# Optimization experiments

Measured on AMD Instinct MI355X. Metric: run time of the kernel, lower is better.

The kernel has to match this reference:

```python
import jax, jax.numpy as jnp
import numpy as np

N_NODES = 100000
N_EDGES = 1600000
IN_FEATS = 128
HEADS = 4
OUT_FEATS = 16


def setup_inputs() -> dict:
    key = jax.random.key(0)
    k1, k2, k3, k4, k5 = jax.random.split(key, 5)
    x = jax.random.normal(k1, (N_NODES, IN_FEATS), dtype=jnp.float32)
    edge_index = jax.random.randint(k2, (2, N_EDGES), 0, N_NODES, dtype=jnp.int64)
    # glorot init scales
    s_w = float(np.sqrt(6.0 / (IN_FEATS + HEADS * OUT_FEATS)))
    s_a = float(np.sqrt(6.0 / (HEADS + OUT_FEATS)))
    W = jax.random.uniform(k3, (HEADS * OUT_FEATS, IN_FEATS), jnp.float32, -s_w, s_w)
    att_i = jax.random.uniform(k4, (1, HEADS, OUT_FEATS), jnp.float32, -s_a, s_a)
    att_j = jax.random.uniform(k5, (1, HEADS, OUT_FEATS), jnp.float32, -s_a, s_a)
    return {"x": x, "edge_index": edge_index, "W": W, "att_i": att_i, "att_j": att_j}


def reference(x, edge_index, W, att_i, att_j):
    N = x.shape[0]
    H, F = att_i.shape[1], att_i.shape[2]
    src = edge_index[0]  # j (source / message sender)
    dst = edge_index[1]  # i (destination / softmax segment)
    # linear projection: [N, H, F]
    h = (x @ W.T).reshape(N, H, F)
    h_j = h[src]  # [E, H, F]
    h_i = h[dst]  # [E, H, F]
    # attention logits per edge per head
    alpha = jnp.einsum('ehf,khf->eh', h_i, att_i) + jnp.einsum('ehf,khf->eh', h_j, att_j)
    alpha = jax.nn.leaky_relu(alpha, negative_slope=0.01)
    # segment softmax over incoming edges of each destination node
    amax = jax.ops.segment_max(alpha, dst, num_segments=N)  # [N, H]
    amax = jnp.where(jnp.isfinite(amax), amax, 0.0)
    ex = jnp.exp(alpha - amax[dst])
    denom = jax.ops.segment_sum(ex, dst, num_segments=N)  # [N, H]
    alpha = ex / (denom[dst] + 1e-16)
    # weighted scatter-sum aggregation
    msg = h_j * alpha[:, :, None]  # [E, H, F]
    out = jax.ops.segment_sum(msg, dst, num_segments=N)  # [N, H, F]
    return out.reshape(N, H * F)
```

## Files before the change

### kernel.cpp

```cpp
#include <hip/hip_runtime.h>

typedef __attribute__((ext_vector_type(8))) short short8;
typedef __attribute__((ext_vector_type(4))) float f32x4;

#define N_NODES 100000
#define N_EDGES 1600000
#define IN_F 128
#define OUT_ALL 64
#define HEADS 4
#define OUT_F 16
#define NTILES (N_NODES / 16)
#define BIN_BLOCKS 250
#define EPB (N_EDGES / BIN_BLOCKS)
#define TOTAL_BLOCKS 2048
#define PROJ_BLOCKS (TOTAL_BLOCKS - BIN_BLOCKS)
#define SLICE_SHIFT 8
#define SLICE_NODES 256
#define NSLICES ((N_NODES + SLICE_NODES - 1) / SLICE_NODES)
#define SEG_CAP 4608
#define QUARTER_NODES 64
#define SORT_CAP 1280

static __device__ __forceinline__ ushort f2bf(float f) {
    unsigned u = __float_as_uint(f);
    return (ushort)((u + 0x7FFF + ((u >> 16) & 1)) >> 16);
}
static __device__ __forceinline__ float bf2f(ushort b) {
    return __uint_as_float(((unsigned)b) << 16);
}
static __device__ __forceinline__ float lrelu(float v) {
    return v > 0.f ? v : 0.01f * v;
}
static __device__ __forceinline__ short8 pack_bf16x8(float4 f0, float4 f1) {
    union { unsigned u[4]; short8 s; } r;
    asm("v_cvt_pk_bf16_f32 %0, %1, %2" : "=v"(r.u[0]) : "v"(f0.x), "v"(f0.y));
    asm("v_cvt_pk_bf16_f32 %0, %1, %2" : "=v"(r.u[1]) : "v"(f0.z), "v"(f0.w));
    asm("v_cvt_pk_bf16_f32 %0, %1, %2" : "=v"(r.u[2]) : "v"(f1.x), "v"(f1.y));
    asm("v_cvt_pk_bf16_f32 %0, %1, %2" : "=v"(r.u[3]) : "v"(f1.z), "v"(f1.w));
    return r.s;
}

__global__ __launch_bounds__(256) void prep_kernel(
    const float* __restrict__ W, const float* __restrict__ att_i,
    const float* __restrict__ att_j, float* __restrict__ wiwj,
    int* __restrict__ scursor)
{
    int idx = blockIdx.x * 256 + threadIdx.x;
    if (idx < NSLICES) scursor[idx] = 0;
    if (idx >= IN_F * 8) return;
    int k = idx >> 3, c = idx & 7;
    int h = c & 3;
    const float* att = (c < 4) ? att_i : att_j;
    float s = 0.f;
    #pragma unroll
    for (int f = 0; f < 16; ++f)
        s += W[(size_t)(h * 16 + f) * IN_F + k] * att[h * OUT_F + f];
    wiwj[k * 8 + c] = s;
}

__global__ __launch_bounds__(256) void proj_bin_kernel(
    const float* __restrict__ x, const float* __restrict__ W,
    const float* __restrict__ wiwj, const int* __restrict__ ei,
    ushort* __restrict__ hb, float* __restrict__ ai, float* __restrict__ aj,
    int* __restrict__ scursor, int2* __restrict__ seg)
{
    __shared__ int cnt[NSLICES];
    __shared__ int gbase[NSLICES];
    __shared__ int run[NSLICES];
    __shared__ __align__(16) ushort xsb[16][144];

    if (blockIdx.x < BIN_BLOCKS) {
        int base = blockIdx.x * EPB;
        const int4* __restrict__ srcp = (const int4*)(ei + base);
        const int4* __restrict__ dstp = (const int4*)(ei + N_EDGES + base);
        for (int s = threadIdx.x; s < NSLICES; s += 256) { cnt[s] = 0; run[s] = 0; }
        __syncthreads();
        for (int i = threadIdx.x; i < EPB / 4; i += 256) {
            int4 d = dstp[i];
            atomicAdd(&cnt[d.x >> SLICE_SHIFT], 1);
            atomicAdd(&cnt[d.y >> SLICE_SHIFT], 1);
            atomicAdd(&cnt[d.z >> SLICE_SHIFT], 1);
            atomicAdd(&cnt[d.w >> SLICE_SHIFT], 1);
        }
        __syncthreads();
        for (int s = threadIdx.x; s < NSLICES; s += 256) {
            int c = cnt[s];
            gbase[s] = c ? atomicAdd(&scursor[s], c) : 0;
        }
        __syncthreads();
        for (int i = threadIdx.x; i < EPB / 4; i += 256) {
            int4 sv = srcp[i];
            int4 dv = dstp[i];
            int ss, p;
            ss = dv.x >> SLICE_SHIFT; p = gbase[ss] + atomicAdd(&run[ss], 1);
            if (p < SEG_CAP) seg[(size_t)ss * SEG_CAP + p] = make_int2(sv.x, dv.x);
            ss = dv.y >> SLICE_SHIFT; p = gbase[ss] + atomicAdd(&run[ss], 1);
            if (p < SEG_CAP) seg[(size_t)ss * SEG_CAP + p] = make_int2(sv.y, dv.y);
            ss = dv.z >> SLICE_SHIFT; p = gbase[ss] + atomicAdd(&run[ss], 1);
            if (p < SEG_CAP) seg[(size_t)ss * SEG_CAP + p] = make_int2(sv.z, dv.z);
            ss = dv.w >> SLICE_SHIFT; p = gbase[ss] + atomicAdd(&run[ss], 1);
            if (p < SEG_CAP) seg[(size_t)ss * SEG_CAP + p] = make_int2(sv.w, dv.w);
        }
        return;
    }

    int bproj = blockIdx.x - BIN_BLOCKS;
    const int nproj = PROJ_BLOCKS;

    int w   = threadIdx.x >> 6;
    int l   = threadIdx.x & 63;
    int col = l & 15;
    int kg  = l >> 4;

    short8 bw[4];
    #pragma unroll
    for (int m = 0; m < 4; ++m) {
        const float* wp = W + (size_t)(w * 16 + col) * IN_F + m * 32 + kg * 8;
        float4 f0 = *(const float4*)wp;
        float4 f1 = *(const float4*)(wp + 4);
        bw[m] = pack_bf16x8(f0, f1);
    }
    short8 bwd[4];
    #pragma unroll
    for (int m = 0; m < 4; ++m) {
        float v[8];
        #pragma unroll
        for (int j = 0; j < 8; ++j)
            v[j] = (col < 8) ? wiwj[(size_t)(m * 32 + kg * 8 + j) * 8 + col] : 0.f;
        bwd[m] = pack_bf16x8(float4{v[0], v[1], v[2], v[3]},
                             float4{v[4], v[5], v[6], v[7]});
    }

    int srow = threadIdx.x >> 4;
    int sc8  = threadIdx.x & 15;

    for (int t = bproj; t < NTILES; t += nproj) {
        int nodeBase = t * 16;

        __syncthreads();
        {
            const float* xp = x + (size_t)(nodeBase + srow) * IN_F + sc8 * 8;
            float4 f0 = *(const float4*)xp;
            float4 f1 = *(const float4*)(xp + 4);
            *(short8*)&xsb[srow][sc8 * 8] = pack_bf16x8(f0, f1);
        }
        __syncthreads();

        short8 a[4];
        #pragma unroll
        for (int m = 0; m < 4; ++m)
            a[m] = *(const short8*)&xsb[col][m * 32 + kg * 8];

        f32x4 acc = {0.f, 0.f, 0.f, 0.f};
        f32x4 accd = {0.f, 0.f, 0.f, 0.f};
        #pragma unroll
        for (int m = 0; m < 4; ++m) {
            acc  = __builtin_amdgcn_mfma_f32_16x16x32_bf16(a[m], bw[m],  acc,  0, 0, 0);
            accd = __builtin_amdgcn_mfma_f32_16x16x32_bf16(a[m], bwd[m], accd, 0, 0, 0);
        }

        #pragma unroll
        for (int r = 0; r < 4; ++r)
            hb[(size_t)(nodeBase + kg * 4 + r) * OUT_ALL + w * 16 + col] = f2bf(acc[r]);

        if (col < 4) {
            #pragma unroll
            for (int r = 0; r < 4; ++r)
                ai[(size_t)(nodeBase + kg * 4 + r) * HEADS + col] = accd[r];
        } else if (col < 8) {
            #pragma unroll
            for (int r = 0; r < 4; ++r)
                aj[(size_t)(nodeBase + kg * 4 + r) * HEADS + (col - 4)] = accd[r];
        }
    }
}

__global__ __launch_bounds__(512) void agg_kernel(
    const int2* __restrict__ seg, const int* __restrict__ scursor,
    const ushort* __restrict__ hb, const float* __restrict__ ai,
    const float* __restrict__ aj, float* __restrict__ out)
{
    __shared__ int staged[SORT_CAP];
    __shared__ int sorted_src[SORT_CAP];
    __shared__ int cnt[QUARTER_NODES];
    __shared__ int run[QUARTER_NODES];
    __shared__ int rowptr[QUARTER_NODES + 1];
    __shared__ int scnt_s;

    int s       = blockIdx.x >> 2;
    int quarter = blockIdx.x & 3;
    int nbase   = (s << SLICE_SHIFT) + quarter * QUARTER_NODES;
    int total = scursor[s]; if (total > SEG_CAP) total = SEG_CAP;
    const int2* sp = seg + (size_t)s * SEG_CAP;

    for (int i = threadIdx.x; i < QUARTER_NODES; i += 512) { cnt[i] = 0; run[i] = 0; }
    if (threadIdx.x == 0) scnt_s = 0;
    __syncthreads();

    int lane = threadIdx.x & 63;
    for (int i = threadIdx.x; i < total; i += 512) {
        int2 e = sp[i];
        int d = e.y & (SLICE_NODES - 1);
        bool m = (d >> 6) == quarter;
        unsigned long long mask = __ballot(m);
        if (mask) {
            int leader = (int)__ffsll((long long)mask) - 1;
            int base = 0;
            if (lane == leader)
                base = atomicAdd(&scnt_s, (int)__popcll(mask));
            base = __shfl(base, leader, 64);
            if (m) {
                int p = base + (int)__popcll(mask & ((1ull << lane) - 1ull));
                if (p < SORT_CAP) staged[p] = (e.x << 6) | (d & 63);
                atomicAdd(&cnt[d & 63], 1);
            }
        }
    }
    __syncthreads();

    if (threadIdx.x < 64) {
        int l = threadIdx.x;
        int v = cnt[l];
        int inc = v;
        #pragma unroll
        for (int d = 1; d < 64; d <<= 1) {
            int t = __shfl_up(inc, d, 64);
            if (l >= d) inc += t;
        }
        rowptr[l] = inc - v;
        if (l == 63) rowptr[64] = inc;
    }
    __syncthreads();

    int scnt = scnt_s; if (scnt > SORT_CAP) scnt = SORT_CAP;
    for (int i = threadIdx.x; i < scnt; i += 512) {
        int v = staged[i];
        int lb = v & 63;
        int p = rowptr[lb] + atomicAdd(&run[lb], 1);
        if (p < SORT_CAP) sorted_src[p] = (int)((unsigned)v >> 6);
    }
    __syncthreads();

    int g    = threadIdx.x >> 3;
    int sub  = threadIdx.x & 7;
    int head = sub >> 1;
    int node = nbase + g;
    if (node >= N_NODES) return;
    int beg = rowptr[g], end = rowptr[g + 1];
    if (end > SORT_CAP) end = SORT_CAP;
    float aiv = ai[(size_t)node * HEADS + head];
    float acc[8] = {0.f, 0.f, 0.f, 0.f, 0.f, 0.f, 0.f, 0.f};
    float den = 0.f;

    int k = beg;
    for (; k + 4 <= end; k += 4) {
        int s0 = sorted_src[k + 0];
        int s1 = sorted_src[k + 1];
        int s2 = sorted_src[k + 2];
        int s3 = sorted_src[k + 3];
        float aj0 = aj[(size_t)s0 * HEADS + head];
        float aj1 = aj[(size_t)s1 * HEADS + head];
        float aj2 = aj[(size_t)s2 * HEADS + head];
        float aj3 = aj[(size_t)s3 * HEADS + head];
        short8 h0 = *(const short8*)(hb + (size_t)s0 * OUT_ALL + sub * 8);
        short8 h1 = *(const short8*)(hb + (size_t)s1 * OUT_ALL + sub * 8);
        short8 h2 = *(const short8*)(hb + (size_t)s2 * OUT_ALL + sub * 8);
        short8 h3 = *(const short8*)(hb + (size_t)s3 * OUT_ALL + sub * 8);
        float e0 = __expf(lrelu(aiv + aj0));
        float e1 = __expf(lrelu(aiv + aj1));
        float e2 = __expf(lrelu(aiv + aj2));
        float e3 = __expf(lrelu(aiv + aj3));
        den += (e0 + e1) + (e2 + e3);
        #pragma unroll
        for (int q = 0; q < 8; ++q)
            acc[q] += e0 * bf2f((ushort)h0[q]) + e1 * bf2f((ushort)h1[q]) +
                      e2 * bf2f((ushort)h2[q]) + e3 * bf2f((ushort)h3[q]);
    }
    for (; k < end; ++k) {
        int src = sorted_src[k];
        float ex = __expf(lrelu(aiv + aj[(size_t)src * HEADS + head]));
        den += ex;
        short8 hv = *(const short8*)(hb + (size_t)src * OUT_ALL + sub * 8);
        #pragma unroll
        for (int q = 0; q < 8; ++q)
            acc[q] += ex * bf2f((ushort)hv[q]);
    }

    float inv = 1.0f / (den + 1e-16f);
    float4 o0 = {acc[0] * inv, acc[1] * inv, acc[2] * inv, acc[3] * inv};
    float4 o1 = {acc[4] * inv, acc[5] * inv, acc[6] * inv, acc[7] * inv};
    float* op = out + (size_t)node * OUT_ALL + sub * 8;
    *(float4*)op = o0;
    *(float4*)(op + 4) = o1;
}

extern "C" void kernel_launch(void* const* d_in, const int* in_sizes, int n_in,
                              void* d_out, int out_size, void* d_ws, size_t ws_size,
                              hipStream_t stream) {
    const float* x     = (const float*)d_in[0];
    const int*   ei    = (const int*)d_in[1];
    const float* W     = (const float*)d_in[2];
    const float* att_i = (const float*)d_in[3];
    const float* att_j = (const float*)d_in[4];
    float* out = (float*)d_out;

    char* ws = (char*)d_ws;
    size_t off = 0;
    auto alloc = [&](size_t bytes) {
        void* p = ws + off;
        off += (bytes + 255) & ~(size_t)255;
        return p;
    };
    ushort* hb      = (ushort*)alloc((size_t)N_NODES * OUT_ALL * 2);
    float*  ai      = (float*)alloc((size_t)N_NODES * HEADS * 4);
    float*  aj      = (float*)alloc((size_t)N_NODES * HEADS * 4);
    float*  wiwj    = (float*)alloc((size_t)IN_F * 8 * 4);
    int*    scursor = (int*)alloc((size_t)NSLICES * 4);
    int2*   seg     = (int2*)alloc((size_t)NSLICES * SEG_CAP * 8);

    prep_kernel<<<(IN_F * 8 + 255) / 256, 256, 0, stream>>>(
        W, att_i, att_j, wiwj, scursor);
    proj_bin_kernel<<<TOTAL_BLOCKS, 256, 0, stream>>>(
        x, W, wiwj, ei, hb, ai, aj, scursor, seg);
    agg_kernel<<<NSLICES * 4, 512, 0, stream>>>(seg, scursor, hb, ai, aj, out);
}
```

Before: 88.58 us.

## Make aggregation a persistent kernel with atomic work queue; prefetch next x tile

New measurement: 104.2 us. 17.6% more time.

```diff
diff --git a/kernel.cpp b/kernel.cpp
--- a/kernel.cpp
+++ b/kernel.cpp
@@ -20,6 +20,8 @@
 #define SEG_CAP 4608
 #define QUARTER_NODES 64
 #define SORT_CAP 1280
+#define NCHUNKS (NSLICES * 4)
+#define AGG_BLOCKS 1024
 
 static __device__ __forceinline__ ushort f2bf(float f) {
     unsigned u = __float_as_uint(f);
@@ -43,10 +45,11 @@
 __global__ __launch_bounds__(256) void prep_kernel(
     const float* __restrict__ W, const float* __restrict__ att_i,
     const float* __restrict__ att_j, float* __restrict__ wiwj,
-    int* __restrict__ scursor)
+    int* __restrict__ scursor, int* __restrict__ workctr)
 {
     int idx = blockIdx.x * 256 + threadIdx.x;
     if (idx < NSLICES) scursor[idx] = 0;
+    if (idx == NSLICES) *workctr = 0;
     if (idx >= IN_F * 8) return;
     int k = idx >> 3, c = idx & 7;
     int h = c & 3;
@@ -134,22 +137,31 @@
     int srow = threadIdx.x >> 4;
     int sc8  = threadIdx.x & 15;
 
+    float4 p0 = {0,0,0,0}, p1 = {0,0,0,0};
+    if (bproj < NTILES) {
+        const float* xp = x + (size_t)(bproj * 16 + srow) * IN_F + sc8 * 8;
+        p0 = *(const float4*)xp;
+        p1 = *(const float4*)(xp + 4);
+    }
+
     for (int t = bproj; t < NTILES; t += nproj) {
         int nodeBase = t * 16;
 
         __syncthreads();
-        {
-            const float* xp = x + (size_t)(nodeBase + srow) * IN_F + sc8 * 8;
-            float4 f0 = *(const float4*)xp;
-            float4 f1 = *(const float4*)(xp + 4);
-            *(short8*)&xsb[srow][sc8 * 8] = pack_bf16x8(f0, f1);
-        }
+        *(short8*)&xsb[srow][sc8 * 8] = pack_bf16x8(p0, p1);
         __syncthreads();
 
         short8 a[4];
         #pragma unroll
         for (int m = 0; m < 4; ++m)
             a[m] = *(const short8*)&xsb[col][m * 32 + kg * 8];
+
+        int tn = t + nproj;
+        if (tn < NTILES) {
+            const float* xp = x + (size_t)(tn * 16 + srow) * IN_F + sc8 * 8;
+            p0 = *(const float4*)xp;
+            p1 = *(const float4*)(xp + 4);
+        }
 
         f32x4 acc = {0.f, 0.f, 0.f, 0.f};
         f32x4 accd = {0.f, 0.f, 0.f, 0.f};
@@ -178,7 +190,8 @@
 __global__ __launch_bounds__(512) void agg_kernel(
     const int2* __restrict__ seg, const int* __restrict__ scursor,
     const ushort* __restrict__ hb, const float* __restrict__ ai,
-    const float* __restrict__ aj, float* __restrict__ out)
+    const float* __restrict__ aj, float* __restrict__ out,
+    int* __restrict__ workctr)
 {
     __shared__ int staged[SORT_CAP];
     __shared__ int sorted_src[SORT_CAP];
@@ -186,112 +199,123 @@
     __shared__ int run[QUARTER_NODES];
     __shared__ int rowptr[QUARTER_NODES + 1];
     __shared__ int scnt_s;
-
-    int s       = blockIdx.x >> 2;
-    int quarter = blockIdx.x & 3;
-    int nbase   = (s << SLICE_SHIFT) + quarter * QUARTER_NODES;
-    int total = scursor[s]; if (total > SEG_CAP) total = SEG_CAP;
-    const int2* sp = seg + (size_t)s * SEG_CAP;
-
-    for (int i = threadIdx.x; i < QUARTER_NODES; i += 512) { cnt[i] = 0; run[i] = 0; }
-    if (threadIdx.x == 0) scnt_s = 0;
-    __syncthreads();
+    __shared__ int chunk_s;
 
     int lane = threadIdx.x & 63;
-    for (int i = threadIdx.x; i < total; i += 512) {
-        int2 e = sp[i];
-        int d = e.y & (SLICE_NODES - 1);
-        bool m = (d >> 6) == quarter;
-        unsigned long long mask = __ballot(m);
-        if (mask) {
-            int leader = (int)__ffsll((long long)mask) - 1;
-            int base = 0;
-            if (lane == leader)
-                base = atomicAdd(&scnt_s, (int)__popcll(mask));
-            base = __shfl(base, leader, 64);
-            if (m) {
-                int p = base + (int)__popcll(mask & ((1ull << lane) - 1ull));
-                if (p < SORT_CAP) staged[p] = (e.x << 6) | (d & 63);
-                atomicAdd(&cnt[d & 63], 1);
+
+    for (;;) {
+        if (threadIdx.x == 0) chunk_s = atomicAdd(workctr, 1);
+        __syncthreads();
+        int chunk = chunk_s;
+        if (chunk >= NCHUNKS) return;
+
+        int s       = chunk >> 2;
+        int quarter = chunk & 3;
+        int nbase   = (s << SLICE_SHIFT) + quarter * QUARTER_NODES;
+        int total = scursor[s]; if (total > SEG_CAP) total = SEG_CAP;
+        const int2* sp = seg + (size_t)s * SEG_CAP;
+
+        for (int i = threadIdx.x; i < QUARTER_NODES; i += 512) { cnt[i] = 0; run[i] = 0; }
+        if (threadIdx.x == 0) scnt_s = 0;
+        __syncthreads();
+
+        for (int i = threadIdx.x; i < total; i += 512) {
+            int2 e = sp[i];
+            int d = e.y & (SLICE_NODES - 1);
+            bool m = (d >> 6) == quarter;
+            unsigned long long mask = __ballot(m);
+            if (mask) {
+                int leader = (int)__ffsll((long long)mask) - 1;
+                int base = 0;
+                if (lane == leader)
+                    base = atomicAdd(&scnt_s, (int)__popcll(mask));
+                base = __shfl(base, leader, 64);
+                if (m) {
+                    int p = base + (int)__popcll(mask & ((1ull << lane) - 1ull));
+                    if (p < SORT_CAP) staged[p] = (e.x << 6) | (d & 63);
+                    atomicAdd(&cnt[d & 63], 1);
+                }
             }
         }
-    }
-    __syncthreads();
-
-    if (threadIdx.x < 64) {
-        int l = threadIdx.x;
-        int v = cnt[l];
-        int inc = v;
-        #pragma unroll
-        for (int d = 1; d < 64; d <<= 1) {
-            int t = __shfl_up(inc, d, 64);
-            if (l >= d) inc += t;
-        }
-        rowptr[l] = inc - v;
-        if (l == 63) rowptr[64] = inc;
-    }
-    __syncthreads();
-
-    int scnt = scnt_s; if (scnt > SORT_CAP) scnt = SORT_CAP;
-    for (int i = threadIdx.x; i < scnt; i += 512) {
-        int v = staged[i];
-        int lb = v & 63;
-        int p = rowptr[lb] + atomicAdd(&run[lb], 1);
-        if (p < SORT_CAP) sorted_src[p] = (int)((unsigned)v >> 6);
-    }
-    __syncthreads();
-
-    int g    = threadIdx.x >> 3;
-    int sub  = threadIdx.x & 7;
-    int head = sub >> 1;
-    int node = nbase + g;
-    if (node >= N_NODES) return;
-    int beg = rowptr[g], end = rowptr[g + 1];
-    if (end > SORT_CAP) end = SORT_CAP;
-    float aiv = ai[(size_t)node * HEADS + head];
-    float acc[8] = {0.f, 0.f, 0.f, 0.f, 0.f, 0.f, 0.f, 0.f};
-    float den = 0.f;
-
-    int k = beg;
-    for (; k + 4 <= end; k += 4) {
-        int s0 = sorted_src[k + 0];
-        int s1 = sorted_src[k + 1];
-        int s2 = sorted_src[k + 2];
-        int s3 = sorted_src[k + 3];
-        float aj0 = aj[(size_t)s0 * HEADS + head];
-        float aj1 = aj[(size_t)s1 * HEADS + head];
-        float aj2 = aj[(size_t)s2 * HEADS + head];
-        float aj3 = aj[(size_t)s3 * HEADS + head];
-        short8 h0 = *(const short8*)(hb + (size_t)s0 * OUT_ALL + sub * 8);
-        short8 h1 = *(const short8*)(hb + (size_t)s1 * OUT_ALL + sub * 8);
-        short8 h2 = *(const short8*)(hb + (size_t)s2 * OUT_ALL + sub * 8);
-        short8 h3 = *(const short8*)(hb + (size_t)s3 * OUT_ALL + sub * 8);
-        float e0 = __expf(lrelu(aiv + aj0));
-        float e1 = __expf(lrelu(aiv + aj1));
-        float e2 = __expf(lrelu(aiv + aj2));
-        float e3 = __expf(lrelu(aiv + aj3));
-        den += (e0 + e1) + (e2 + e3);
-        #pragma unroll
-        for (int q = 0; q < 8; ++q)
-            acc[q] += e0 * bf2f((ushort)h0[q]) + e1 * bf2f((ushort)h1[q]) +
-                      e2 * bf2f((ushort)h2[q]) + e3 * bf2f((ushort)h3[q]);
-    }
-    for (; k < end; ++k) {
-        int src = sorted_src[k];
-        float ex = __expf(lrelu(aiv + aj[(size_t)src * HEADS + head]));
-        den += ex;
-        short8 hv = *(const short8*)(hb + (size_t)src * OUT_ALL + sub * 8);
-        #pragma unroll
-        for (int q = 0; q < 8; ++q)
-            acc[q] += ex * bf2f((ushort)hv[q]);
-    }
-
-    float inv = 1.0f / (den + 1e-16f);
-    float4 o0 = {acc[0] * inv, acc[1] * inv, acc[2] * inv, acc[3] * inv};
-    float4 o1 = {acc[4] * inv, acc[5] * inv, acc[6] * inv, acc[7] * inv};
-    float* op = out + (size_t)node * OUT_ALL + sub * 8;
-    *(float4*)op = o0;
-    *(float4*)(op + 4) = o1;
+        __syncthreads();
+
+        if (threadIdx.x < 64) {
+            int l = threadIdx.x;
+            int v = cnt[l];
+            int inc = v;
+            #pragma unroll
+            for (int d = 1; d < 64; d <<= 1) {
+                int t = __shfl_up(inc, d, 64);
+                if (l >= d) inc += t;
+            }
+            rowptr[l] = inc - v;
+            if (l == 63) rowptr[64] = inc;
+        }
+        __syncthreads();
+
+        int scnt = scnt_s; if (scnt > SORT_CAP) scnt = SORT_CAP;
+        for (int i = threadIdx.x; i < scnt; i += 512) {
+            int v = staged[i];
+            int lb = v & 63;
+            int p = rowptr[lb] + atomicAdd(&run[lb], 1);
+            if (p < SORT_CAP) sorted_src[p] = (int)((unsigned)v >> 6);
+        }
+        __syncthreads();
+
+        int g    = threadIdx.x >> 3;
+        int sub  = threadIdx.x & 7;
+        int head = sub >> 1;
+        int node = nbase + g;
+        if (node < N_NODES) {
+            int beg = rowptr[g], end = rowptr[g + 1];
+            if (end > SORT_CAP) end = SORT_CAP;
+            float aiv = ai[(size_t)node * HEADS + head];
+            float acc[8] = {0.f, 0.f, 0.f, 0.f, 0.f, 0.f, 0.f, 0.f};
+            float den = 0.f;
+
+            int k = beg;
+            for (; k + 4 <= end; k += 4) {
+                int s0 = sorted_src[k + 0];
+                int s1 = sorted_src[k + 1];
+                int s2 = sorted_src[k + 2];
+                int s3 = sorted_src[k + 3];
+                float aj0 = aj[(size_t)s0 * HEADS + head];
+                float aj1 = aj[(size_t)s1 * HEADS + head];
+                float aj2 = aj[(size_t)s2 * HEADS + head];
+                float aj3 = aj[(size_t)s3 * HEADS + head];
+                short8 h0 = *(const short8*)(hb + (size_t)s0 * OUT_ALL + sub * 8);
+                short8 h1 = *(const short8*)(hb + (size_t)s1 * OUT_ALL + sub * 8);
+                short8 h2 = *(const short8*)(hb + (size_t)s2 * OUT_ALL + sub * 8);
+                short8 h3 = *(const short8*)(hb + (size_t)s3 * OUT_ALL + sub * 8);
+                float e0 = __expf(lrelu(aiv + aj0));
+                float e1 = __expf(lrelu(aiv + aj1));
+                float e2 = __expf(lrelu(aiv + aj2));
+                float e3 = __expf(lrelu(aiv + aj3));
+                den += (e0 + e1) + (e2 + e3);
+                #pragma unroll
+                for (int q = 0; q < 8; ++q)
+                    acc[q] += e0 * bf2f((ushort)h0[q]) + e1 * bf2f((ushort)h1[q]) +
+                              e2 * bf2f((ushort)h2[q]) + e3 * bf2f((ushort)h3[q]);
+            }
+            for (; k < end; ++k) {
+                int src = sorted_src[k];
+                float ex = __expf(lrelu(aiv + aj[(size_t)src * HEADS + head]));
+                den += ex;
+                short8 hv = *(const short8*)(hb + (size_t)src * OUT_ALL + sub * 8);
+                #pragma unroll
+                for (int q = 0; q < 8; ++q)
+                    acc[q] += ex * bf2f((ushort)hv[q]);
+            }
+
+            float inv = 1.0f / (den + 1e-16f);
+            float4 o0 = {acc[0] * inv, acc[1] * inv, acc[2] * inv, acc[3] * inv};
+            float4 o1 = {acc[4] * inv, acc[5] * inv, acc[6] * inv, acc[7] * inv};
+            float* op = out + (size_t)node * OUT_ALL + sub * 8;
+            *(float4*)op = o0;
+            *(float4*)(op + 4) = o1;
+        }
+        __syncthreads();
+    }
 }
 
 extern "C" void kernel_launch(void* const* d_in, const int* in_sizes, int n_in,
@@ -315,12 +339,14 @@
     float*  ai      = (float*)alloc((size_t)N_NODES * HEADS * 4);
     float*  aj      = (float*)alloc((size_t)N_NODES * HEADS * 4);
     float*  wiwj    = (float*)alloc((size_t)IN_F * 8 * 4);
-    int*    scursor = (int*)alloc((size_t)NSLICES * 4);
+    int*    scursor = (int*)alloc((size_t)(NSLICES + 64) * 4);
+    int*    workctr = scursor + NSLICES;
     int2*   seg     = (int2*)alloc((size_t)NSLICES * SEG_CAP * 8);
 
     prep_kernel<<<(IN_F * 8 + 255) / 256, 256, 0, stream>>>(
-        W, att_i, att_j, wiwj, scursor);
+        W, att_i, att_j, wiwj, scursor, workctr);
     proj_bin_kernel<<<TOTAL_BLOCKS, 256, 0, stream>>>(
         x, W, wiwj, ei, hb, ai, aj, scursor, seg);
-    agg_kernel<<<NSLICES * 4, 512, 0, stream>>>(seg, scursor, hb, ai, aj, out);
-}
+    agg_kernel<<<AGG_BLOCKS, 512, 0, stream>>>(
+        seg, scursor, hb, ai, aj, out, workctr);
+}
```
